# Performance work log

Hardware: AMD Instinct MI355X
Metric: run time of the kernel (lower is better)

## Reference

```python
import jax, jax.numpy as jnp
import numpy as np

MAX_DISP = 4                    # R: max displacement of the correlation window
D = 2 * MAX_DISP + 1            # window side -> D*D = 81 offset channels


def setup_inputs() -> dict:
    key = jax.random.key(0)
    k1, k2 = jax.random.split(key)
    B, C, H, W = 16, 256, 96, 96
    reference_features = jax.random.normal(k1, (B, D * D, H, W), dtype=jnp.float32)
    query_features = jax.random.normal(k2, (B, C, H, W), dtype=jnp.float32)
    return {"reference_features": reference_features, "query_features": query_features}


def reference(reference_features, query_features):
    # reference_features: [B, D*D, H, W] correlation volume (weights per spatial offset)
    # query_features:     [B, C, H, W]  feature map
    # out[b,c,y,x] = sum_{dy,dx in [-R,R]} corr[b, idx(dy,dx), y-dy, x-dx] * feat[b,c,y-dy,x-dx]
    # i.e. the adjoint of local correlation: scatter-accumulate across shifted windows.
    B, D2, H, W = reference_features.shape
    C = query_features.shape[1]
    R = MAX_DISP
    # Padded accumulator so every shifted write stays in-bounds (zero padding semantics).
    acc = jnp.zeros((B, C, H + 2 * R, W + 2 * R), dtype=query_features.dtype)
    for idx in range(D2):  # fixed small offset set (81), not a data-dim loop
        dy = idx // D - R
        dx = idx % D - R
        w = reference_features[:, idx:idx + 1] * query_features  # [B, C, H, W]
        acc = acc.at[:, :, R + dy:R + dy + H, R + dx:R + dx + W].add(w)
    return acc[:, :, R:R + H, R:R + W]
```

## Files before the change

### kernel.cpp

```cpp
#include <hip/hip_runtime.h>


#define RR 4
#define DD 9
#define D2 81
#define Bn 16
#define Cn 256
#define Hn 96
#define Wn 96
#define HWn (Hn*Wn)
#define NTH 512
#define KW  104
#define MW  32

typedef __attribute__((ext_vector_type(8))) short bf16x8;
typedef __attribute__((ext_vector_type(4))) float f32x4;

__device__ __forceinline__ uint cvt_pk(float lo, float hi) {
    uint r;
    asm("v_cvt_pk_bf16_f32 %0, %1, %2" : "=v"(r) : "v"(lo), "v"(hi));
    return r;
}
__device__ __forceinline__ ushort f2bf(float f) {
    uint u = __float_as_uint(f);
    return (ushort)((u + 0x7FFFu + ((u >> 16) & 1u)) >> 16);
}

#define PREP_MB (Bn*Hn)
#define PREP_FT 2560
__global__ __launch_bounds__(384)
void prep_all_kernel(const float* __restrict__ feat, const float* __restrict__ corr,
                     ushort* __restrict__ featb, ushort* __restrict__ mband)
{
    if (blockIdx.x < PREP_MB) {
        const int s  = blockIdx.x;
        const int sy = s % Hn, b = s / Hn;
        const float* cb = corr + (size_t)b * D2 * HWn + (size_t)sy * Wn;
        const int t   = threadIdx.x;
        const int x   = t >> 2, oct = t & 3;
        const int kb  = (x >= 80) ? 72 : (x & ~15);
        ushort* mbase = mband + ((size_t)s * DD) * (Wn * MW) + x * MW + oct * 8;
        #pragma unroll 1
        for (int kdy = 0; kdy < DD; ++kdy) {
            ushort v[8];
            #pragma unroll
            for (int i = 0; i < 8; ++i) {
                int o   = oct * 8 + i;
                int sxp = kb + o;
                int kdx = x + 2 * RR - sxp;
                float f = 0.f;
                if (kdx >= 0 && kdx < DD && sxp >= RR && sxp < Wn + RR)
                    f = cb[(size_t)(kdy * DD + kdx) * HWn + (sxp - RR)];
                v[i] = f2bf(f);
            }
            *reinterpret_cast<uint4*>(mbase + (size_t)kdy * (Wn * MW)) =
                make_uint4((uint)v[0] | ((uint)v[1] << 16), (uint)v[2] | ((uint)v[3] << 16),
                           (uint)v[4] | ((uint)v[5] << 16), (uint)v[6] | ((uint)v[7] << 16));
        }
    } else {
        const int n8 = Bn * Cn * HWn / 8;
        const float4* src = reinterpret_cast<const float4*>(feat);
        uint4* dst = reinterpret_cast<uint4*>(featb);
        for (int i = (blockIdx.x - PREP_MB) * 384 + threadIdx.x; i < n8; i += PREP_FT * 384) {
            float4 a = src[2 * i], c = src[2 * i + 1];
            dst[i] = make_uint4(cvt_pk(a.x, a.y), cvt_pk(a.z, a.w), cvt_pk(c.x, c.y), cvt_pk(c.z, c.w));
        }
    }
}

__global__ __launch_bounds__(NTH, 2)
void corrT18_kernel(const ushort* __restrict__ featb, const ushort* __restrict__ mband,
                    float* __restrict__ out)
{
    __shared__ ushort A_sh[Cn][KW];
    __shared__ ushort M_sh[2][Wn][MW];

    int bid = blockIdx.x;
    int L   = (bid & 7) * 192 + (bid >> 3);
    int y   = L % Hn;
    int b   = L / Hn;

    const int tid  = threadIdx.x;
    const int lane = tid & 63;
    const int wid  = tid >> 6;
    const int mrow = lane & 15;
    const int kq   = lane >> 4;
    const int kgrp = kq << 3;

    for (int i = tid; i < Cn; i += NTH) {
        *reinterpret_cast<uint2*>(&A_sh[i][0])   = make_uint2(0u, 0u);
        *reinterpret_cast<uint2*>(&A_sh[i][100]) = make_uint2(0u, 0u);
    }
    __syncthreads();

    const int klo = max(0, y - (Hn - 1 - RR));
    const int khi = min(DD - 1, y + RR);

    const int ac  = tid >> 1;
    const int seg = tid & 1;
    const ushort* fb_base = featb + (((size_t)b * Cn + ac) * Hn) * (size_t)Wn + seg * 48;

    const int mwrow = tid >> 2;
    const int mwp   = ((tid & 3) << 2) ^ (((mwrow >> 1) & 3) << 2);
    const int mwidx = mwrow * 4 + (mwp >> 2);

    {
        const int sy = y + RR - klo;
        const uint4* src = reinterpret_cast<const uint4*>(fb_base + (size_t)sy * Wn);
        #pragma unroll
        for (int i = 0; i < 6; ++i) {
            uint4 v = src[i];
            uint2* d = reinterpret_cast<uint2*>(&A_sh[ac][4 + seg * 48 + i * 8]);
            d[0] = make_uint2(v.x, v.y);
            d[1] = make_uint2(v.z, v.w);
        }
        const ushort* ms = mband + (((size_t)b * Hn + sy) * DD + klo) * (size_t)(Wn * MW);
        if (tid < 384)
            reinterpret_cast<uint4*>(&M_sh[0][0][0])[mwidx] = reinterpret_cast<const uint4*>(ms)[tid];
    }
    __syncthreads();

    f32x4 acc[2][6];
    #pragma unroll
    for (int ct = 0; ct < 2; ++ct)
        #pragma unroll
        for (int t6 = 0; t6 < 6; ++t6)
            acc[ct][t6] = (f32x4){0.f, 0.f, 0.f, 0.f};

    #pragma unroll 1
    for (int kk = klo; kk <= khi; ++kk) {
        const int pb = (kk - klo) & 1;
        const bool vn = (kk + 1 <= khi);
        const int syn = y + RR - (kk + 1);

        uint4 a0, a1, a2, a3, a4, a5;
        uint4 mvv = make_uint4(0u, 0u, 0u, 0u);
        if (vn) {
            const uint4* src = reinterpret_cast<const uint4*>(fb_base + (size_t)syn * Wn);
            a0 = src[0]; a1 = src[1]; a2 = src[2]; a3 = src[3]; a4 = src[4]; a5 = src[5];
            const ushort* ms = mband + (((size_t)b * Hn + syn) * DD + (kk + 1)) * (size_t)(Wn * MW);
            if (tid < 384) mvv = reinterpret_cast<const uint4*>(ms)[tid];
        }

        #pragma unroll
        for (int t6 = 0; t6 < 6; ++t6) {
            const int kb = (t6 == 5) ? 72 : t6 * 16;
            const int mr = t6 * 16 + mrow;
            const int mp = kgrp ^ (((mr >> 1) & 3) << 3);
            uint4 bw = *reinterpret_cast<const uint4*>(&M_sh[pb][mr][mp]);
            bf16x8 bfr = *reinterpret_cast<bf16x8*>(&bw);
            #pragma unroll
            for (int ct = 0; ct < 2; ++ct) {
                bf16x8 afr = *reinterpret_cast<const bf16x8*>(&A_sh[wid * 32 + ct * 16 + mrow][kb + kgrp]);
                acc[ct][t6] = __builtin_amdgcn_mfma_f32_16x16x32_bf16(afr, bfr, acc[ct][t6], 0, 0, 0);
            }
        }
        __syncthreads();

        if (vn) {
            uint2* d0 = reinterpret_cast<uint2*>(&A_sh[ac][4 + seg * 48]);
            d0[0] = make_uint2(a0.x, a0.y); d0[1] = make_uint2(a0.z, a0.w);
            d0[2] = make_uint2(a1.x, a1.y); d0[3] = make_uint2(a1.z, a1.w);
            d0[4] = make_uint2(a2.x, a2.y); d0[5] = make_uint2(a2.z, a2.w);
            d0[6] = make_uint2(a3.x, a3.y); d0[7] = make_uint2(a3.z, a3.w);
            d0[8] = make_uint2(a4.x, a4.y); d0[9] = make_uint2(a4.z, a4.w);
            d0[10] = make_uint2(a5.x, a5.y); d0[11] = make_uint2(a5.z, a5.w);
            if (tid < 384)
                reinterpret_cast<uint4*>(&M_sh[pb ^ 1][0][0])[mwidx] = mvv;
        }
        __syncthreads();
    }

    const int csub = kq << 2;
    #pragma unroll
    for (int ct = 0; ct < 2; ++ct)
        #pragma unroll
        for (int t6 = 0; t6 < 6; ++t6)
            #pragma unroll
            for (int r = 0; r < 4; ++r)
                out[(((size_t)b * Cn + wid * 32 + ct * 16 + csub + r) * Hn + y) * Wn + t6 * 16 + mrow]
                    = acc[ct][t6][r];
}

#define NTXf 12
#define NTCf 32
#define NTHf (NTXf*NTCf)
#define LWf  100
#define LW4f (LWf/4)
__global__ __launch_bounds__(NTHf, 6)
void corrT8_kernel(const float* __restrict__ corr, const float* __restrict__ feat,
                   float* __restrict__ out)
{
    __shared__ float lds[D2 * LWf];
    int bid = blockIdx.x;
    int sw  = (bid & 7) * (gridDim.x >> 3) + (bid >> 3);
    int cg  = sw & 3;
    int y   = (sw >> 2) % Hn;
    int b   = sw / (4 * Hn);
    const int tid = threadIdx.x;
    const float* corrb = corr + (size_t)b * D2 * HWn;
    for (int idx = tid; idx < D2 * LW4f; idx += NTHf) {
        int row = idx / LW4f, c4 = idx - row * LW4f;
        int kdy = row / DD, kdx = row - kdy * DD;
        int sy  = y + RR - kdy;
        float4 v = make_float4(0.f, 0.f, 0.f, 0.f);
        if (sy >= 0 && sy < Hn) {
            const float* src = corrb + (size_t)row * HWn + sy * Wn;
            #pragma unroll
            for (int e = 0; e < 4; ++e) {
                int sx = c4 * 4 + e - kdx;
                if (sx >= 0 && sx < Wn) (&v.x)[e] = src[sx];
            }
        }
        *reinterpret_cast<float4*>(&lds[row * LWf + c4 * 4]) = v;
    }
    __syncthreads();
    const int tx = tid % NTXf, tc = tid / NTXf;
    const int x0 = tx * 8, c0 = cg * 64 + tc * 2;
    const float* featp = feat + ((size_t)b * Cn + c0) * HWn;
    float acc[2][8] = {};
    const int klo = max(0, y - (Hn - 1 - RR)), khi = min(DD - 1, y + RR);
    #pragma unroll 1
    for (int kdy = klo; kdy <= khi; ++kdy) {
        int sy = y + RR - kdy;
        float f[2][16];
        const float* frow = featp + sy * Wn + x0 - RR;
        #pragma unroll
        for (int c = 0; c < 2; ++c) {
            const float* p = frow + (size_t)c * HWn;
            float4 f0 = (tx == 0) ? make_float4(0,0,0,0) : *reinterpret_cast<const float4*>(p);
            float4 f1 = *reinterpret_cast<const float4*>(p + 4);
            float4 f2 = *reinterpret_cast<const float4*>(p + 8);
            float4 f3 = (tx == NTXf-1) ? make_float4(0,0,0,0) : *reinterpret_cast<const float4*>(p + 12);
            f[c][0]=f0.x; f[c][1]=f0.y; f[c][2]=f0.z; f[c][3]=f0.w;
            f[c][4]=f1.x; f[c][5]=f1.y; f[c][6]=f1.z; f[c][7]=f1.w;
            f[c][8]=f2.x; f[c][9]=f2.y; f[c][10]=f2.z; f[c][11]=f2.w;
            f[c][12]=f3.x; f[c][13]=f3.y; f[c][14]=f3.z; f[c][15]=f3.w;
        }
        const float4* base = reinterpret_cast<const float4*>(lds) + (tx * 2 + 1) + kdy * DD * LW4f;
        float4 ca = base[0], cb = base[1];
        #pragma unroll
        for (int kdx = 0; kdx < DD; ++kdx) {
            float4 na = ca, nb = cb;
            if (kdx < DD - 1) { na = base[(kdx+1)*LW4f]; nb = base[(kdx+1)*LW4f + 1]; }
            float cv[8] = {ca.x, ca.y, ca.z, ca.w, cb.x, cb.y, cb.z, cb.w};
            #pragma unroll
            for (int c = 0; c < 2; ++c)
                #pragma unroll
                for (int j = 0; j < 8; ++j)
                    acc[c][j] = fmaf(cv[j], f[c][j + 8 - kdx], acc[c][j]);
            ca = na; cb = nb;
        }
    }
    float* ob = out + ((size_t)b * Cn + c0) * HWn + (size_t)y * Wn + x0;
    #pragma unroll
    for (int c = 0; c < 2; ++c) {
        *reinterpret_cast<float4*>(ob + (size_t)c * HWn)     = make_float4(acc[c][0], acc[c][1], acc[c][2], acc[c][3]);
        *reinterpret_cast<float4*>(ob + (size_t)c * HWn + 4) = make_float4(acc[c][4], acc[c][5], acc[c][6], acc[c][7]);
    }
}

extern "C" void kernel_launch(void* const* d_in, const int* in_sizes, int n_in,
                              void* d_out, int out_size, void* d_ws, size_t ws_size,
                              hipStream_t stream)
{
    const float* corr = (const float*)d_in[0];
    const float* feat = (const float*)d_in[1];
    float* out = (float*)d_out;

    const size_t needF = (size_t)Bn * Cn * HWn * 2;
    const size_t needM = (size_t)Bn * Hn * DD * Wn * MW * 2;

    if (ws_size >= needF + needM) {
        ushort* featb = (ushort*)d_ws;
        ushort* mband = (ushort*)((char*)d_ws + needF);
        prep_all_kernel<<<PREP_MB + PREP_FT, 384, 0, stream>>>(feat, corr, featb, mband);
        corrT18_kernel<<<Bn * Hn, NTH, 0, stream>>>(featb, mband, out);
    } else {
        corrT8_kernel<<<Bn * Hn * 4, NTHf, 0, stream>>>(corr, feat, out);
    }
}
```

Baseline: 198.0 us.

## Retile correlation-transpose kernel over 8 output rows and 32 channels per block

Each block now covers an 8-row by 32-channel output tile instead of one row by all 256 channels. It streams 16 input feature rows through a small double-buffered LDS tile, and each wave owns one output row. The banded weight matrix is read straight from global memory into MFMA B-fragments instead of being staged in LDS. LDS use drops sharply and the launch bound rises to 4 blocks per CU for more occupancy. The cost is uncached per-wave global loads of the weight band and idle waves on boundary steps.

```diff
diff --git a/kernel.cpp b/kernel.cpp
--- a/kernel.cpp
+++ b/kernel.cpp
@@ -9,8 +9,6 @@
 #define Hn 96
 #define Wn 96
 #define HWn (Hn*Wn)
-#define NTH 512
-#define KW  104
 #define MW  32
 
 typedef __attribute__((ext_vector_type(8))) short bf16x8;
@@ -68,17 +66,18 @@
     }
 }
 
-__global__ __launch_bounds__(NTH, 2)
-void corrT18_kernel(const ushort* __restrict__ featb, const ushort* __restrict__ mband,
+__global__ __launch_bounds__(512, 4)
+void corrT19_kernel(const ushort* __restrict__ featb, const ushort* __restrict__ mband,
                     float* __restrict__ out)
 {
-    __shared__ ushort A_sh[Cn][KW];
-    __shared__ ushort M_sh[2][Wn][MW];
+    __shared__ ushort A_sh[2][32][104];
 
     int bid = blockIdx.x;
     int L   = (bid & 7) * 192 + (bid >> 3);
-    int y   = L % Hn;
-    int b   = L / Hn;
+    int cg  = L & 7;
+    int yt  = (L >> 3) % 12;
+    int b   = L / 96;
+    const int y0 = yt * 8, c0 = cg * 32;
 
     const int tid  = threadIdx.x;
     const int lane = tid & 63;
@@ -87,36 +86,26 @@
     const int kq   = lane >> 4;
     const int kgrp = kq << 3;
 
-    for (int i = tid; i < Cn; i += NTH) {
-        *reinterpret_cast<uint2*>(&A_sh[i][0])   = make_uint2(0u, 0u);
-        *reinterpret_cast<uint2*>(&A_sh[i][100]) = make_uint2(0u, 0u);
-    }
-    __syncthreads();
-
-    const int klo = max(0, y - (Hn - 1 - RR));
-    const int khi = min(DD - 1, y + RR);
-
-    const int ac  = tid >> 1;
-    const int seg = tid & 1;
-    const ushort* fb_base = featb + (((size_t)b * Cn + ac) * Hn) * (size_t)Wn + seg * 48;
-
-    const int mwrow = tid >> 2;
-    const int mwp   = ((tid & 3) << 2) ^ (((mwrow >> 1) & 3) << 2);
-    const int mwidx = mwrow * 4 + (mwp >> 2);
+    if (tid < 64) {
+        int bf = tid >> 5, row = tid & 31;
+        *reinterpret_cast<uint2*>(&A_sh[bf][row][0])   = make_uint2(0u, 0u);
+        *reinterpret_cast<uint2*>(&A_sh[bf][row][100]) = make_uint2(0u, 0u);
+    }
+
+    const bool stager = (tid < 192);
+    const int  srow   = stager ? (tid / 6) : 0;
+    const int  sseg   = tid % 6;
+    const ushort* fbase = featb + (((size_t)b * Cn + c0 + srow) * Hn) * (size_t)Wn + sseg * 16;
 
     {
-        const int sy = y + RR - klo;
-        const uint4* src = reinterpret_cast<const uint4*>(fb_base + (size_t)sy * Wn);
-        #pragma unroll
-        for (int i = 0; i < 6; ++i) {
-            uint4 v = src[i];
-            uint2* d = reinterpret_cast<uint2*>(&A_sh[ac][4 + seg * 48 + i * 8]);
-            d[0] = make_uint2(v.x, v.y);
-            d[1] = make_uint2(v.z, v.w);
-        }
-        const ushort* ms = mband + (((size_t)b * Hn + sy) * DD + klo) * (size_t)(Wn * MW);
-        if (tid < 384)
-            reinterpret_cast<uint4*>(&M_sh[0][0][0])[mwidx] = reinterpret_cast<const uint4*>(ms)[tid];
+        const int sy = y0 - 4;
+        if (stager && sy >= 0) {
+            const uint4* p = reinterpret_cast<const uint4*>(fbase + (size_t)sy * Wn);
+            uint4 v0 = p[0], v1 = p[1];
+            uint2* d = reinterpret_cast<uint2*>(&A_sh[0][srow][4 + sseg * 16]);
+            d[0] = make_uint2(v0.x, v0.y); d[1] = make_uint2(v0.z, v0.w);
+            d[2] = make_uint2(v1.x, v1.y); d[3] = make_uint2(v1.z, v1.w);
+        }
     }
     __syncthreads();
 
@@ -128,49 +117,44 @@
             acc[ct][t6] = (f32x4){0.f, 0.f, 0.f, 0.f};
 
     #pragma unroll 1
-    for (int kk = klo; kk <= khi; ++kk) {
-        const int pb = (kk - klo) & 1;
-        const bool vn = (kk + 1 <= khi);
-        const int syn = y + RR - (kk + 1);
-
-        uint4 a0, a1, a2, a3, a4, a5;
-        uint4 mvv = make_uint4(0u, 0u, 0u, 0u);
-        if (vn) {
-            const uint4* src = reinterpret_cast<const uint4*>(fb_base + (size_t)syn * Wn);
-            a0 = src[0]; a1 = src[1]; a2 = src[2]; a3 = src[3]; a4 = src[4]; a5 = src[5];
-            const ushort* ms = mband + (((size_t)b * Hn + syn) * DD + (kk + 1)) * (size_t)(Wn * MW);
-            if (tid < 384) mvv = reinterpret_cast<const uint4*>(ms)[tid];
-        }
-
-        #pragma unroll
-        for (int t6 = 0; t6 < 6; ++t6) {
-            const int kb = (t6 == 5) ? 72 : t6 * 16;
-            const int mr = t6 * 16 + mrow;
-            const int mp = kgrp ^ (((mr >> 1) & 3) << 3);
-            uint4 bw = *reinterpret_cast<const uint4*>(&M_sh[pb][mr][mp]);
-            bf16x8 bfr = *reinterpret_cast<bf16x8*>(&bw);
-            #pragma unroll
-            for (int ct = 0; ct < 2; ++ct) {
-                bf16x8 afr = *reinterpret_cast<const bf16x8*>(&A_sh[wid * 32 + ct * 16 + mrow][kb + kgrp]);
-                acc[ct][t6] = __builtin_amdgcn_mfma_f32_16x16x32_bf16(afr, bfr, acc[ct][t6], 0, 0, 0);
+    for (int s = 0; s < 16; ++s) {
+        const int pb = s & 1;
+
+        const int syn = y0 - 4 + s + 1;
+        uint4 v0, v1;
+        const bool doSt = stager && (s < 15) && (syn >= 0) && (syn < Hn);
+        if (doSt) {
+            const uint4* p = reinterpret_cast<const uint4*>(fbase + (size_t)syn * Wn);
+            v0 = p[0]; v1 = p[1];
+        }
+
+        const int sy  = y0 - 4 + s;
+        const int kdy = wid + (DD - 1) - s;
+        if (kdy >= 0 && kdy < DD && sy >= 0 && sy < Hn) {
+            const ushort* ms = mband + (((size_t)b * Hn + sy) * DD + kdy) * (size_t)(Wn * MW)
+                               + mrow * MW + kgrp;
+            #pragma unroll
+            for (int t6 = 0; t6 < 6; ++t6) {
+                const int kb = (t6 == 5) ? 72 : t6 * 16;
+                uint4 bw = *reinterpret_cast<const uint4*>(ms + t6 * 16 * MW);
+                bf16x8 bfr = *reinterpret_cast<bf16x8*>(&bw);
+                #pragma unroll
+                for (int ct = 0; ct < 2; ++ct) {
+                    bf16x8 afr = *reinterpret_cast<const bf16x8*>(&A_sh[pb][ct * 16 + mrow][kb + kgrp]);
+                    acc[ct][t6] = __builtin_amdgcn_mfma_f32_16x16x32_bf16(afr, bfr, acc[ct][t6], 0, 0, 0);
+                }
             }
         }
+
+        if (doSt) {
+            uint2* d = reinterpret_cast<uint2*>(&A_sh[pb ^ 1][srow][4 + sseg * 16]);
+            d[0] = make_uint2(v0.x, v0.y); d[1] = make_uint2(v0.z, v0.w);
+            d[2] = make_uint2(v1.x, v1.y); d[3] = make_uint2(v1.z, v1.w);
+        }
         __syncthreads();
-
-        if (vn) {
-            uint2* d0 = reinterpret_cast<uint2*>(&A_sh[ac][4 + seg * 48]);
-            d0[0] = make_uint2(a0.x, a0.y); d0[1] = make_uint2(a0.z, a0.w);
-            d0[2] = make_uint2(a1.x, a1.y); d0[3] = make_uint2(a1.z, a1.w);
-            d0[4] = make_uint2(a2.x, a2.y); d0[5] = make_uint2(a2.z, a2.w);
-            d0[6] = make_uint2(a3.x, a3.y); d0[7] = make_uint2(a3.z, a3.w);
-            d0[8] = make_uint2(a4.x, a4.y); d0[9] = make_uint2(a4.z, a4.w);
-            d0[10] = make_uint2(a5.x, a5.y); d0[11] = make_uint2(a5.z, a5.w);
-            if (tid < 384)
-                reinterpret_cast<uint4*>(&M_sh[pb ^ 1][0][0])[mwidx] = mvv;
-        }
-        __syncthreads();
-    }
-
+    }
+
+    const int y = y0 + wid;
     const int csub = kq << 2;
     #pragma unroll
     for (int ct = 0; ct < 2; ++ct)
@@ -178,7 +162,7 @@
         for (int t6 = 0; t6 < 6; ++t6)
             #pragma unroll
             for (int r = 0; r < 4; ++r)
-                out[(((size_t)b * Cn + wid * 32 + ct * 16 + csub + r) * Hn + y) * Wn + t6 * 16 + mrow]
+                out[(((size_t)b * Cn + c0 + ct * 16 + csub + r) * Hn + y) * Wn + t6 * 16 + mrow]
                     = acc[ct][t6][r];
 }
 
@@ -275,7 +259,7 @@
         ushort* featb = (ushort*)d_ws;
         ushort* mband = (ushort*)((char*)d_ws + needF);
         prep_all_kernel<<<PREP_MB + PREP_FT, 384, 0, stream>>>(feat, corr, featb, mband);
-        corrT18_kernel<<<Bn * Hn, NTH, 0, stream>>>(featb, mband, out);
+        corrT19_kernel<<<Bn * Hn, 512, 0, stream>>>(featb, mband, out);
     } else {
         corrT8_kernel<<<Bn * Hn * 4, NTHf, 0, stream>>>(corr, feat, out);
     }
```

Measured after the change: 201.5 us. About the same (+1.8%).
